# Kernel optimization log

Measured on AMD Instinct MI355X. Metric: run time of the kernel, lower is better.

Reference implementation:

```python
import jax, jax.numpy as jnp
import numpy as np

GAMMA = 0.99
RHO_THRESHOLD = 1.0
C_THRESHOLD = 1.0
BASELINE_LOSS_SCALING = 0.5
ENT_COEFF = 0.01
PPO_CLIP = 0.2


def setup_inputs() -> dict:
    key = jax.random.key(0)
    ks = jax.random.split(key, 7)
    T, B, A = 512, 8192, 2
    return {
        "prob": jax.random.uniform(ks[0], (T, B, A), dtype=jnp.float32),
        "action_prob": jax.random.uniform(ks[1], (T, B, A), dtype=jnp.float32),
        "v": jax.random.normal(ks[2], (T, B), dtype=jnp.float32),
        "next_v": jax.random.normal(ks[3], (T, B), dtype=jnp.float32),
        "reward": jax.random.normal(ks[4], (T, B), dtype=jnp.float32),
        "action": jax.random.randint(ks[5], (T, B), 0, 2, dtype=jnp.int32),
        "done": jax.random.randint(ks[6], (T, B), 0, 2, dtype=jnp.int32),
    }


def _log_prob(p, a):
    # torch.distributions.Categorical normalizes unnormalized probs
    logp = jnp.log(p) - jnp.log(p.sum(-1, keepdims=True))  # [T,B,A]
    return jnp.take_along_axis(logp, a[..., None].astype(jnp.int32), axis=-1)[..., 0]


def reference(prob, action_prob, v, next_v, reward, action, done):
    done_f = done.astype(v.dtype)  # [T,B]
    logp = _log_prob(prob, action)
    logp_act = _log_prob(action_prob, action)
    ratio = jnp.exp(logp - logp_act)  # [T,B]

    clipped_rho = jnp.minimum(ratio, RHO_THRESHOLD)
    clipped_c = jnp.minimum(ratio, C_THRESHOLD)
    deltas = clipped_rho * (reward + (1.0 - done_f) * GAMMA * next_v - v)

    # V-trace backward recurrence over time (dim 0), vectorized over batch
    def step(next_vtrace, xs):
        v_t, d_t, c_t, rho_t, r_t, nv_t, dn_t = xs
        vt = v_t + d_t + GAMMA * c_t * (next_vtrace - nv_t) * (1.0 - dn_t)
        adv = rho_t * (r_t + GAMMA * next_vtrace * (1.0 - dn_t) - v_t)
        return vt, (vt, adv)

    _, (vtrace, adv) = jax.lax.scan(
        step, next_v[-1],
        (v, deltas, clipped_c, clipped_rho, reward, next_v, done_f),
        reverse=True)

    vtrace = jax.lax.stop_gradient(vtrace)  # .detach() in original
    adv = jax.lax.stop_gradient(adv)

    critic_loss = BASELINE_LOSS_SCALING * jnp.mean((v - vtrace) ** 2)
    surr1 = ratio * adv
    surr2 = jnp.clip(ratio, 1.0 - PPO_CLIP, 1.0 + PPO_CLIP) * adv
    actor_loss = -jnp.minimum(surr1, surr2).mean()

    # entropy is logged but NOT included in total_loss in the original
    total_loss = actor_loss + critic_loss
    return total_loss
```

## Files before the change

### kernel.cpp

```cpp
#include <hip/hip_runtime.h>

#define T_DIM 512
#define B_DIM 8192
#define GB 16
#define NC 64
#define LC 8
#define BLOCK (GB * NC)
#define GRID (B_DIM / GB)
#define GAMMA 0.99f

__launch_bounds__(BLOCK, 8)
__global__ void vtrace_main(const float* __restrict__ prob,
                            const float* __restrict__ aprob,
                            const float* __restrict__ v,
                            const float* __restrict__ nv,
                            const float* __restrict__ rw,
                            const int* __restrict__ act,
                            const int* __restrict__ dnn,
                            float* __restrict__ ws,
                            float* __restrict__ out) {
    __shared__ float Sc[NC][GB];
    __shared__ float Mc[NC][GB];
    __shared__ float Cin[NC][GB];
    __shared__ float red[32];

    const int tid = threadIdx.x;
    const int bl  = tid & (GB - 1);
    const int c   = tid >> 4;
    const int b   = blockIdx.x * GB + bl;
    const int t0  = c * LC;

    float rsA[LC], pA[LC], vA[LC];
    float S = 0.0f, M = 1.0f;

    const float2* __restrict__ prob2  = (const float2*)prob;
    const float2* __restrict__ aprob2 = (const float2*)aprob;

#pragma unroll
    for (int i = LC - 1; i >= 0; --i) {
        const size_t idx = (size_t)(t0 + i) * B_DIM + b;
        float2 pr = prob2[idx];
        float2 qr = aprob2[idx];
        float vv  = v[idx];
        float rr  = rw[idx];
        int   a   = act[idx];
        int   d   = dnn[idx];

        float pa    = a ? pr.y : pr.x;
        float qa    = a ? qr.y : qr.x;
        float ratio = (pa * (qr.x + qr.y)) / ((pr.x + pr.y) * qa);
        float rho   = fminf(ratio, 1.0f);
        float m     = d ? 0.0f : GAMMA * rho;
        float p     = rho * (rr - vv);

        rsA[i] = d ? -ratio : ratio;
        pA[i]  = p;
        vA[i]  = vv;
        S = (vv + p) + m * S;
        M = m * M;
    }

    Sc[c][bl] = S;
    Mc[c][bl] = M;
    __syncthreads();

    if (tid < GB) {
        float carry = nv[(size_t)(T_DIM - 1) * B_DIM + blockIdx.x * GB + tid];
        for (int cc = NC - 1; cc >= 0; --cc) {
            Cin[cc][tid] = carry;
            carry = Sc[cc][tid] + Mc[cc][tid] * carry;
        }
    }
    __syncthreads();

    float carry  = Cin[c][bl];
    float critic = 0.0f, msum = 0.0f;
#pragma unroll
    for (int i = LC - 1; i >= 0; --i) {
        float rs  = rsA[i];
        float r_  = fabsf(rs);
        float m   = (rs > 0.0f) ? GAMMA * fminf(r_, 1.0f) : 0.0f;
        float adv = pA[i] + m * carry;
        carry     = adv + vA[i];
        critic += adv * adv;
        float rc = fminf(fmaxf(r_, 0.8f), 1.2f);
        msum += fminf(r_ * adv, rc * adv);
    }

#pragma unroll
    for (int off = 32; off > 0; off >>= 1) {
        critic += __shfl_down(critic, off, 64);
        msum   += __shfl_down(msum, off, 64);
    }
    const int wave = tid >> 6;
    if ((tid & 63) == 0) { red[wave] = critic; red[16 + wave] = msum; }
    __syncthreads();

    if (tid == 0) {
        float cs = 0.0f, ms = 0.0f;
#pragma unroll
        for (int w = 0; w < 16; ++w) { cs += red[w]; ms += red[16 + w]; }
        atomicAdd(&ws[0], cs);
        atomicAdd(&ws[1], ms);
        __threadfence();
        unsigned* cnt = (unsigned*)(ws + 2);
        unsigned ticket = atomicAdd(cnt, 1u);
        if (ticket == GRID - 1) {
            __threadfence();
            float c_tot = atomicAdd(&ws[0], 0.0f);
            float m_tot = atomicAdd(&ws[1], 0.0f);
            const float invN = 1.0f / (float)((size_t)T_DIM * B_DIM);
            out[0] = 0.5f * c_tot * invN - m_tot * invN;
        }
    }
}

extern "C" void kernel_launch(void* const* d_in, const int* in_sizes, int n_in,
                              void* d_out, int out_size, void* d_ws, size_t ws_size,
                              hipStream_t stream) {
    const float* prob  = (const float*)d_in[0];
    const float* aprob = (const float*)d_in[1];
    const float* v     = (const float*)d_in[2];
    const float* nv    = (const float*)d_in[3];
    const float* rw    = (const float*)d_in[4];
    const int*   act   = (const int*)d_in[5];
    const int*   dnn   = (const int*)d_in[6];
    float* ws  = (float*)d_ws;
    float* out = (float*)d_out;

    hipMemsetAsync(ws, 0, 12, stream);
    vtrace_main<<<GRID, BLOCK, 0, stream>>>(prob, aprob, v, nv, rw, act, dnn,
                                            ws, out);
}
```

Baseline: 189.3 us.

## Shrink per-block batch tile and stage per-step values in shared memory

Reduces the batch tile to 8 columns with 128 time chunks of 4 steps. Per-step ratio, partial value and v are stored in LDS instead of registers. The carry scan reuses the Sc buffer in place and is unrolled, and indices switch to 32-bit with fma forms. This aims to cut register pressure and raise occupancy, at the cost of narrower 32-byte coalesced segments, a longer serial carry scan and more LDS use.

```diff
diff --git a/kernel.cpp b/kernel.cpp
--- a/kernel.cpp
+++ b/kernel.cpp
@@ -2,9 +2,9 @@
 
 #define T_DIM 512
 #define B_DIM 8192
-#define GB 16
-#define NC 64
-#define LC 8
+#define GB 8
+#define NC 128
+#define LC 4
 #define BLOCK (GB * NC)
 #define GRID (B_DIM / GB)
 #define GAMMA 0.99f
@@ -19,26 +19,25 @@
                             const int* __restrict__ dnn,
                             float* __restrict__ ws,
                             float* __restrict__ out) {
-    __shared__ float Sc[NC][GB];
-    __shared__ float Mc[NC][GB];
-    __shared__ float Cin[NC][GB];
-    __shared__ float red[32];
+    __shared__ float2 RS[LC][BLOCK];
+    __shared__ float  VV[LC][BLOCK];
+    __shared__ float  Sc[NC][GB];
+    __shared__ float  Mc[NC][GB];
+    __shared__ float  red[32];
 
     const int tid = threadIdx.x;
     const int bl  = tid & (GB - 1);
-    const int c   = tid >> 4;
+    const int c   = tid >> 3;
     const int b   = blockIdx.x * GB + bl;
     const int t0  = c * LC;
-
-    float rsA[LC], pA[LC], vA[LC];
-    float S = 0.0f, M = 1.0f;
 
     const float2* __restrict__ prob2  = (const float2*)prob;
     const float2* __restrict__ aprob2 = (const float2*)aprob;
 
+    float S = 0.0f, M = 1.0f;
 #pragma unroll
     for (int i = LC - 1; i >= 0; --i) {
-        const size_t idx = (size_t)(t0 + i) * B_DIM + b;
+        const int idx = (t0 + i) * B_DIM + b;
         float2 pr = prob2[idx];
         float2 qr = aprob2[idx];
         float vv  = v[idx];
@@ -51,38 +50,41 @@
         float ratio = (pa * (qr.x + qr.y)) / ((pr.x + pr.y) * qa);
         float rho   = fminf(ratio, 1.0f);
         float m     = d ? 0.0f : GAMMA * rho;
-        float p     = rho * (rr - vv);
+        float s     = fmaf(rho, rr - vv, vv);
 
-        rsA[i] = d ? -ratio : ratio;
-        pA[i]  = p;
-        vA[i]  = vv;
-        S = (vv + p) + m * S;
+        RS[i][tid] = make_float2(d ? -ratio : ratio, s);
+        VV[i][tid] = vv;
+        S = fmaf(m, S, s);
         M = m * M;
     }
-
     Sc[c][bl] = S;
     Mc[c][bl] = M;
     __syncthreads();
 
     if (tid < GB) {
-        float carry = nv[(size_t)(T_DIM - 1) * B_DIM + blockIdx.x * GB + tid];
+        float carry = nv[(T_DIM - 1) * B_DIM + blockIdx.x * GB + tid];
+#pragma unroll 8
         for (int cc = NC - 1; cc >= 0; --cc) {
-            Cin[cc][tid] = carry;
-            carry = Sc[cc][tid] + Mc[cc][tid] * carry;
+            float s = Sc[cc][tid];
+            float m = Mc[cc][tid];
+            Sc[cc][tid] = carry;
+            carry = fmaf(m, carry, s);
         }
     }
     __syncthreads();
 
-    float carry  = Cin[c][bl];
+    float carry  = Sc[c][bl];
     float critic = 0.0f, msum = 0.0f;
 #pragma unroll
     for (int i = LC - 1; i >= 0; --i) {
-        float rs  = rsA[i];
-        float r_  = fabsf(rs);
-        float m   = (rs > 0.0f) ? GAMMA * fminf(r_, 1.0f) : 0.0f;
-        float adv = pA[i] + m * carry;
-        carry     = adv + vA[i];
-        critic += adv * adv;
+        float2 rs_s = RS[i][tid];
+        float  vv   = VV[i][tid];
+        float  r_   = fabsf(rs_s.x);
+        float  m    = (rs_s.x > 0.0f) ? GAMMA * fminf(r_, 1.0f) : 0.0f;
+        float  u    = fmaf(m, carry, rs_s.y);
+        float  adv  = u - vv;
+        carry       = u;
+        critic = fmaf(adv, adv, critic);
         float rc = fminf(fmaxf(r_, 0.8f), 1.2f);
         msum += fminf(r_ * adv, rc * adv);
     }
```

Measured after the change: 233.3 us. 23.3% more time.
